# Optimization experiments

Measured on AMD Instinct MI355X. Metric: run time of the kernel, lower is better.

The kernel has to match this reference:

```python
import jax, jax.numpy as jnp
import numpy as np

STEP = 256  # samples per frame index step (start = index * 256)


def setup_inputs() -> dict:
    key = jax.random.key(0)
    ks = jax.random.split(key, 6)
    B, E, N, D, R = 64, 8, 32768, 128, 16
    events = jax.random.normal(ks[0], (B, E, N), dtype=jnp.float32) * 0.1
    indices = jax.random.randint(ks[1], (B, E), 0, N // STEP)  # frame offsets
    g = jax.random.normal(ks[2], (B, D), dtype=jnp.float32)
    rooms = jax.random.normal(ks[3], (R, N), dtype=jnp.float32) * 0.05
    w_room = jax.random.normal(ks[4], (D, R), dtype=jnp.float32) * 0.05
    b_room = jnp.zeros((R,), dtype=jnp.float32)
    w_mix = jax.random.normal(ks[5], (D, 1), dtype=jnp.float32) * 0.05
    b_mix = jnp.zeros((1,), dtype=jnp.float32)
    return {"events": events, "indices": indices, "g": g, "rooms": rooms,
            "w_room": w_room, "b_room": b_room, "w_mix": w_mix, "b_mix": b_mix}


def reference(events, indices, g, rooms, w_room, b_room, w_mix, b_mix):
    B, E, N = events.shape
    # --- dynamic-offset overlap-add scatter into a 2N buffer ---
    starts = indices.astype(jnp.int32) * STEP              # [B, E]
    pos = starts[:, :, None] + jnp.arange(N, dtype=jnp.int32)  # [B, E, N]
    buf = jnp.zeros((B, 2 * N), dtype=events.dtype)
    buf = buf.at[jnp.arange(B)[:, None, None], pos].add(events)
    dry = buf[:, :N]                                        # [B, N]
    # --- neural reverb: softmax room mixture, FFT convolution ---
    room_w = jax.nn.softmax(g @ w_room + b_room, axis=-1)   # [B, R]
    kernel = room_w @ rooms                                 # [B, N]
    L = 2 * N
    wet = jnp.fft.irfft(jnp.fft.rfft(dry, n=L) * jnp.fft.rfft(kernel, n=L), n=L)[:, :N]
    # --- wet/dry mix and peak normalization ---
    mix = jax.nn.sigmoid(g @ w_mix + b_mix)                 # [B, 1]
    out = mix * wet + (1.0 - mix) * dry                     # [B, N]
    out = out[:, None, :]                                   # [B, 1, N]
    mx = jnp.max(out, axis=-1, keepdims=True)
    return out / (mx + 1e-8)
```

## Files before the change

### kernel.cpp

```cpp
#include <hip/hip_runtime.h>
#include <hip/hip_fp16.h>
#include <math.h>

#define N_T 32768
#define L 65536
#define BATCH 64
#define NPAIR 32
#define NEV 8
#define NROOM 16
#define DGATE 128
#define ROWP 258
#define TWP 65
#define TWP2 33
#define TILE 16384
#define TWO_PI 6.2831853071795864769f
#define INV_L (1.0f / 65536.0f)
#define PW_SCALE (1.0f / 256.0f)
#define COL_SCALE (1.0f / 256.0f)

__device__ __forceinline__ float2 cmul(float2 a, float2 b) {
    return make_float2(a.x * b.x - a.y * b.y, a.x * b.y + a.y * b.x);
}
__device__ __forceinline__ int dr4(int p) {
    return ((p & 3) << 6) | ((p & 12) << 2) | ((p & 48) >> 2) | ((p & 192) >> 6);
}

__device__ __forceinline__ void bf4f(float2& a, float2& b, float2& c, float2& d,
                                     const float2* tw, int f, int q) {
    float2 t0 = make_float2(a.x + c.x, a.y + c.y);
    float2 t1 = make_float2(a.x - c.x, a.y - c.y);
    float2 t2 = make_float2(b.x + d.x, b.y + d.y);
    float2 u  = make_float2(b.x - d.x, b.y - d.y);
    float2 t3 = make_float2(u.y, -u.x);
    a = make_float2(t0.x + t2.x, t0.y + t2.y);
    b = cmul(make_float2(t1.x + t3.x, t1.y + t3.y), tw[f * q]);
    c = cmul(make_float2(t0.x - t2.x, t0.y - t2.y), tw[2 * f * q]);
    d = cmul(make_float2(t1.x - t3.x, t1.y - t3.y), tw[3 * f * q]);
}
__device__ __forceinline__ void bf4i(float2& a, float2& b, float2& c, float2& d,
                                     const float2* tw, int f, int q) {
    float2 w1 = tw[f * q], w2 = tw[2 * f * q], w3 = tw[3 * f * q];
    float2 y0 = a;
    float2 y1 = cmul(b, make_float2(w1.x, -w1.y));
    float2 y2 = cmul(c, make_float2(w2.x, -w2.y));
    float2 y3 = cmul(d, make_float2(w3.x, -w3.y));
    float2 t0 = make_float2(y0.x + y2.x, y0.y + y2.y);
    float2 t2 = make_float2(y0.x - y2.x, y0.y - y2.y);
    float2 t1 = make_float2(y1.x + y3.x, y1.y + y3.y);
    float2 u  = make_float2(y1.x - y3.x, y1.y - y3.y);
    a = make_float2(t0.x + t1.x, t0.y + t1.y);
    b = make_float2(t2.x - u.y, t2.y + u.x);
    c = make_float2(t0.x - t1.x, t0.y - t1.y);
    d = make_float2(t2.x + u.y, t2.y - u.x);
}
__device__ __forceinline__ void bfly4_fwd(float2* A, int a0, int st, const float2* tw, int f, int q) {
    bf4f(A[a0], A[a0 + st], A[a0 + 2 * st], A[a0 + 3 * st], tw, f, q);
}
__device__ __forceinline__ void bfly4_inv(float2* A, int a0, int st, const float2* tw, int f, int q) {
    bf4i(A[a0], A[a0 + st], A[a0 + 2 * st], A[a0 + 3 * st], tw, f, q);
}

__global__ __launch_bounds__(1024) void k_fwd(const float* __restrict__ events,
                                              const int* __restrict__ indices,
                                              const float* __restrict__ rooms,
                                              const float* __restrict__ g,
                                              const float* __restrict__ w_room,
                                              const float* __restrict__ b_room,
                                              __half* __restrict__ dryfh,
                                              __half2* __restrict__ C) {
    __shared__ float2 T[128 * TWP];
    __shared__ float2 tw[256];
    __shared__ float2 fine[256];
    __shared__ float wr_s[NROOM];
    int t = threadIdx.x;
    int a = blockIdx.x >> 2;
    int cg = blockIdx.x & 3;
    int c0 = cg * 64;
    __half2* tile = C + ((size_t)(a * 4 + cg)) * TILE;
    if (t < 256) {
        float sv, cv;
        __sincosf(-TWO_PI * (float)t * (1.0f / 256.0f), &sv, &cv);
        tw[t] = make_float2(cv, sv);
        __sincosf(-TWO_PI * (float)t * INV_L, &sv, &cv);
        fine[t] = make_float2(cv, sv);
    }
    if (t >= 256 && t < 256 + NROOM) {
        int r = t - 256;
        const float* gb = g + a * DGATE;
        float acc = b_room[r];
        for (int d = 0; d < DGATE; d++) acc += gb[d] * w_room[d * NROOM + r];
        wr_s[r] = acc;
    }
    __syncthreads();
    if (t == 0) {
        float m = wr_s[0];
        for (int r = 1; r < NROOM; r++) m = fmaxf(m, wr_s[r]);
        float e[NROOM];
        float s = 0.f;
        for (int r = 0; r < NROOM; r++) { e[r] = expf(wr_s[r] - m); s += e[r]; }
        float inv = 1.f / s;
        for (int r = 0; r < NROOM; r++) wr_s[r] = e[r] * inv;
    }
    __syncthreads();
    float* dtile = (float*)T;
    float* ktile = dtile + 128 * 64;
    {
        int n2 = t >> 3;
        int cc = (t & 7) << 3;
        const float* eb = events + (size_t)a * NEV * N_T;
        const int* ib = indices + a * NEV;
        float4 dA = make_float4(0.f, 0.f, 0.f, 0.f), dB = dA;
#pragma unroll
        for (int e = 0; e < NEV; e++) {
            int s = ib[e];
            if (n2 >= s) {
                const float* er = eb + e * N_T + ((n2 - s) << 8) + c0 + cc;
                float4 vA = *(const float4*)er;
                float4 vB = *(const float4*)(er + 4);
                dA.x += vA.x; dA.y += vA.y; dA.z += vA.z; dA.w += vA.w;
                dB.x += vB.x; dB.y += vB.y; dB.z += vB.z; dB.w += vB.w;
            }
        }
        float4 kA = make_float4(0.f, 0.f, 0.f, 0.f), kB = kA;
#pragma unroll
        for (int r = 0; r < NROOM; r++) {
            float w = wr_s[r];
            const float* rr = rooms + (size_t)r * N_T + (n2 << 8) + c0 + cc;
            float4 vA = *(const float4*)rr;
            float4 vB = *(const float4*)(rr + 4);
            kA.x += w * vA.x; kA.y += w * vA.y; kA.z += w * vA.z; kA.w += w * vA.w;
            kB.x += w * vB.x; kB.y += w * vB.y; kB.z += w * vB.z; kB.w += w * vB.w;
        }
        __half2 hd[4];
        hd[0] = __float22half2_rn(make_float2(dA.x, dA.y));
        hd[1] = __float22half2_rn(make_float2(dA.z, dA.w));
        hd[2] = __float22half2_rn(make_float2(dB.x, dB.y));
        hd[3] = __float22half2_rn(make_float2(dB.z, dB.w));
        *(float4*)(dryfh + (size_t)a * N_T + (n2 << 8) + c0 + cc) = *(float4*)hd;
        *(float4*)&dtile[(n2 << 6) + cc] = dA;
        *(float4*)&dtile[(n2 << 6) + cc + 4] = dB;
        *(float4*)&ktile[(n2 << 6) + cc] = kA;
        *(float4*)&ktile[(n2 << 6) + cc + 4] = kB;
    }
    __syncthreads();
    int j = t >> 6, c = t & 63;
    int n1 = c0 + c;
    float2 r[16];
#pragma unroll
    for (int m = 0; m < 8; m++) {
        int n2 = j + 16 * m;
        r[m] = make_float2(dtile[(n2 << 6) + c], ktile[(n2 << 6) + c]);
    }
#pragma unroll
    for (int m = 8; m < 16; m++) r[m] = make_float2(0.f, 0.f);
#pragma unroll
    for (int m0 = 0; m0 < 4; m0++) bf4f(r[m0], r[m0 + 4], r[m0 + 8], r[m0 + 12], tw, 1, j + 16 * m0);
#pragma unroll
    for (int h = 0; h < 4; h++) bf4f(r[4 * h], r[4 * h + 1], r[4 * h + 2], r[4 * h + 3], tw, 4, j);
    __syncthreads();
    float2 r2[16];
#pragma unroll
    for (int m = 0; m < 8; m++) T[(j + 16 * m) * TWP + c] = r[m];
    __syncthreads();
    if (j < 8) {
#pragma unroll
        for (int jj = 0; jj < 16; jj++) r2[jj] = T[(jj + 16 * j) * TWP + c];
    }
    __syncthreads();
#pragma unroll
    for (int m = 8; m < 16; m++) T[(j + 16 * m - 128) * TWP + c] = r[m];
    __syncthreads();
    if (j >= 8) {
#pragma unroll
        for (int jj = 0; jj < 16; jj++) r2[jj] = T[(jj + 16 * (j - 8)) * TWP + c];
    }
#pragma unroll
    for (int q = 0; q < 4; q++) bf4f(r2[q], r2[q + 4], r2[q + 8], r2[q + 12], tw, 16, q);
#pragma unroll
    for (int h = 0; h < 4; h++) bf4f(r2[4 * h], r2[4 * h + 1], r2[4 * h + 2], r2[4 * h + 3], tw, 64, 0);
#pragma unroll
    for (int jj = 0; jj < 16; jj++) {
        int p = jj + 16 * j;
        int k2 = dr4(p);
        int ph = (n1 * k2) & (L - 1);
        float2 w = cmul(tw[ph >> 8], fine[ph & 255]);
        tile[(p << 6) + c] = __float22half2_rn(cmul(r2[jj], w));
    }
}

__device__ __forceinline__ void pw_unit(float2* A, int sJ, int kJ, int sN, int kN) {
    float2 Z0j = A[sJ * ROWP + kJ],       Z0n = A[sN * ROWP + kN];
    float2 Z1j = A[(4 + sJ) * ROWP + kJ], Z1n = A[(4 + sN) * ROWP + kN];
    float2 D0 = make_float2(0.5f * (Z0j.x + Z0n.x), 0.5f * (Z0j.y - Z0n.y));
    float2 K0 = make_float2(0.5f * (Z0j.y + Z0n.y), 0.5f * (Z0n.x - Z0j.x));
    float2 D1 = make_float2(0.5f * (Z1j.x + Z1n.x), 0.5f * (Z1j.y - Z1n.y));
    float2 K1 = make_float2(0.5f * (Z1j.y + Z1n.y), 0.5f * (Z1n.x - Z1j.x));
    float2 W0 = cmul(D0, K0);
    float2 W1 = cmul(D1, K1);
    A[sJ * ROWP + kJ] = make_float2((W0.x - W1.y) * PW_SCALE, (W0.y + W1.x) * PW_SCALE);
    A[sN * ROWP + kN] = make_float2((W0.x + W1.y) * PW_SCALE, (W1.x - W0.y) * PW_SCALE);
}

__global__ void k_rowpw(__half2* __restrict__ C) {
    __shared__ float2 A[8 * ROWP];
    __shared__ float2 tw[192];
    int t = threadIdx.x;
    int p = blockIdx.x >> 6;
    int g = blockIdx.x & 63;
    int rows[4];
    if (g == 0) { rows[0] = 0; rows[1] = 1; rows[2] = 128; rows[3] = 255; }
    else        { rows[0] = 2 * g; rows[1] = 2 * g + 1; rows[2] = 256 - 2 * g; rows[3] = 255 - 2 * g; }
    if (t < 192) {
        float sv, cv;
        __sincosf(-TWO_PI * (float)t * (1.0f / 256.0f), &sv, &cv);
        tw[t] = make_float2(cv, sv);
    }
    __half2* b0 = C + ((size_t)(2 * p) * 4) * TILE;
    __half2* b1 = b0 + 4 * TILE;
    for (int u = t; u < 512; u += 256) {
        int slot = u >> 6;
        int f = (u & 63) << 2;
        int cg = f >> 6, c2 = f & 63;
        const __half2* arr = (slot < 4) ? b0 : b1;
        int grow = dr4(rows[slot & 3]);
        float4 raw = *(const float4*)(arr + cg * TILE + (grow << 6) + c2);
        const __half2* hp = (const __half2*)&raw;
        A[slot * ROWP + f]     = __half22float2(hp[0]);
        A[slot * ROWP + f + 1] = __half22float2(hp[1]);
        A[slot * ROWP + f + 2] = __half22float2(hp[2]);
        A[slot * ROWP + f + 3] = __half22float2(hp[3]);
    }
    __syncthreads();
#pragma unroll
    for (int lm = 8; lm >= 6; lm -= 2) {
        int Q = 1 << (lm - 2), f = 256 >> lm;
        for (int u = t; u < 512; u += 256) {
            int row = u >> 6, qi = u & 63;
            int q = qi & (Q - 1);
            int i0 = ((qi - q) << 2) + q;
            bfly4_fwd(A, row * ROWP + i0, Q, tw, f, q);
        }
        __syncthreads();
    }
#pragma unroll
    for (int lm = 4; lm >= 2; lm -= 2) {
        int Q = 1 << (lm - 2), f = 256 >> lm;
        for (int u = t; u < 512; u += 256) {
            int row = u & 7, qi = u >> 3;
            int q = qi & (Q - 1);
            int i0 = ((qi - q) << 2) + q;
            bfly4_fwd(A, row * ROWP + i0, Q, tw, f, q);
        }
        __syncthreads();
    }
    if (g) {
        pw_unit(A, 0, t, 2, 255 - t);
    } else {
        if (t == 0)      { pw_unit(A, 0, 0, 0, 0); pw_unit(A, 0, 2, 0, 2); }
        else if (t < 128) pw_unit(A, 0, dr4(t), 0, dr4(256 - t));
        else              { int qq = t - 128; pw_unit(A, 2, qq, 2, 255 - qq); }
    }
    pw_unit(A, 1, t, 3, 255 - t);
    __syncthreads();
#pragma unroll
    for (int lm = 2; lm <= 4; lm += 2) {
        int Q = 1 << (lm - 2), f = 256 >> lm;
        int row = t & 3, qi = t >> 2;
        int q = qi & (Q - 1);
        int i0 = ((qi - q) << 2) + q;
        bfly4_inv(A, row * ROWP + i0, Q, tw, f, q);
        __syncthreads();
    }
#pragma unroll
    for (int lm = 6; lm <= 8; lm += 2) {
        int Q = 1 << (lm - 2), f = 256 >> lm;
        int row = t >> 6, qi = t & 63;
        int q = qi & (Q - 1);
        int i0 = ((qi - q) << 2) + q;
        bfly4_inv(A, row * ROWP + i0, Q, tw, f, q);
        __syncthreads();
    }
    {
        int u = t;
        int slot = u >> 6;
        int f = (u & 63) << 2;
        int cg = f >> 6, c2 = f & 63;
        int r = rows[slot];
        __half2 outv[4];
#pragma unroll
        for (int i = 0; i < 4; i++) {
            float2 v = A[slot * ROWP + f + i];
            int ph = ((f + i) * r) & (L - 1);
            float sv, cv;
            __sincosf(TWO_PI * (float)ph * INV_L, &sv, &cv);
            outv[i] = __float22half2_rn(cmul(v, make_float2(cv, sv)));
        }
        *(float4*)(b0 + cg * TILE + (dr4(r) << 6) + c2) = *(float4*)outv;
    }
}

__global__ __launch_bounds__(512) void k_colinv(const __half2* __restrict__ C,
                                                const __half* __restrict__ dryfh,
                                                const float* __restrict__ g,
                                                const float* __restrict__ w_mix,
                                                const float* __restrict__ b_mix,
                                                __half* __restrict__ mixo,
                                                float* __restrict__ partial) {
    __shared__ float2 T[128 * TWP2];
    __shared__ float2 tw[256];
    __shared__ float sm0[8], sm1[8];
    __shared__ float smix[2];
    int t = threadIdx.x;
    int a = blockIdx.x >> 3;
    int cgrp = blockIdx.x & 7;
    int c0 = cgrp * 32;
    const __half2* tile = C + ((size_t)(2 * a * 4 + (c0 >> 6))) * TILE;
    int coff = c0 & 63;
    if (t < 256) {
        float sv, cv;
        __sincosf(-TWO_PI * (float)t * (1.0f / 256.0f), &sv, &cv);
        tw[t] = make_float2(cv, sv);
    }
    if (t >= 256 && t < 258) {
        int bb = 2 * a + (t - 256);
        const float* gb = g + bb * DGATE;
        float acc = b_mix[0];
        for (int d = 0; d < DGATE; d++) acc += gb[d] * w_mix[d];
        smix[t - 256] = 1.f / (1.f + expf(-acc));
    }
    int j = t >> 5, c = t & 31;
    int n1 = c0 + c;
    float2 r[16];
#pragma unroll
    for (int jj = 0; jj < 16; jj++)
        r[jj] = __half22float2(tile[((jj + 16 * j) << 6) + coff + c]);
    __syncthreads();
#pragma unroll
    for (int h = 0; h < 4; h++) bf4i(r[4 * h], r[4 * h + 1], r[4 * h + 2], r[4 * h + 3], tw, 64, 0);
#pragma unroll
    for (int q = 0; q < 4; q++) bf4i(r[q], r[q + 4], r[q + 8], r[q + 12], tw, 16, q);
    float2 r2[16];
    if (j < 8) {
#pragma unroll
        for (int jj = 0; jj < 16; jj++) T[(jj + 16 * j) * TWP2 + c] = r[jj];
    }
    __syncthreads();
#pragma unroll
    for (int m = 0; m < 8; m++) r2[m] = T[(j + 16 * m) * TWP2 + c];
    __syncthreads();
    if (j >= 8) {
#pragma unroll
        for (int jj = 0; jj < 16; jj++) T[(16 * (j - 8) + jj) * TWP2 + c] = r[jj];
    }
    __syncthreads();
#pragma unroll
    for (int m = 8; m < 16; m++) r2[m] = T[(j + 16 * (m - 8)) * TWP2 + c];
#pragma unroll
    for (int h = 0; h < 4; h++) bf4i(r2[4 * h], r2[4 * h + 1], r2[4 * h + 2], r2[4 * h + 3], tw, 4, j);
#pragma unroll
    for (int m0 = 0; m0 < 4; m0++) bf4i(r2[m0], r2[m0 + 4], r2[m0 + 8], r2[m0 + 12], tw, 1, j + 16 * m0);
    int b0 = 2 * a, b1 = 2 * a + 1;
    float mix0 = smix[0], mix1 = smix[1];
    float om0 = 1.f - mix0, om1 = 1.f - mix1;
    const __half* dry0 = dryfh + (size_t)b0 * N_T;
    const __half* dry1 = dryfh + (size_t)b1 * N_T;
    __half* mo0 = mixo + (size_t)b0 * N_T;
    __half* mo1 = mixo + (size_t)b1 * N_T;
    float m0 = -3.4e38f, m1 = -3.4e38f;
#pragma unroll
    for (int m = 0; m < 8; m++) {
        int pos = n1 + ((j + 16 * m) << 8);
        float d0 = __half2float(dry0[pos]), d1 = __half2float(dry1[pos]);
        float o0 = mix0 * (r2[m].x * COL_SCALE) + om0 * d0;
        float o1 = mix1 * (r2[m].y * COL_SCALE) + om1 * d1;
        mo0[pos] = __float2half(o0);
        mo1[pos] = __float2half(o1);
        m0 = fmaxf(m0, o0);
        m1 = fmaxf(m1, o1);
    }
#pragma unroll
    for (int off = 32; off > 0; off >>= 1) {
        m0 = fmaxf(m0, __shfl_down(m0, off));
        m1 = fmaxf(m1, __shfl_down(m1, off));
    }
    if ((t & 63) == 0) { sm0[t >> 6] = m0; sm1[t >> 6] = m1; }
    __syncthreads();
    if (t == 0) {
        float p0 = sm0[0], p1 = sm1[0];
#pragma unroll
        for (int w = 1; w < 8; w++) { p0 = fmaxf(p0, sm0[w]); p1 = fmaxf(p1, sm1[w]); }
        partial[b0 * 8 + cgrp] = p0;
        partial[b1 * 8 + cgrp] = p1;
    }
}

__global__ void k_norm(const __half* __restrict__ mixo, const float* __restrict__ partial,
                       float* __restrict__ out) {
    int blk = blockIdx.x;
    int b = blk >> 5;
    int ch = blk & 31;
    __shared__ float smx;
    if (threadIdx.x < 8) {
        float p = partial[b * 8 + threadIdx.x];
#pragma unroll
        for (int off = 4; off > 0; off >>= 1) p = fmaxf(p, __shfl_down(p, off, 8));
        if (threadIdx.x == 0) smx = p;
    }
    __syncthreads();
    float inv = 1.f / (smx + 1e-8f);
    size_t base = (size_t)b * N_T + ch * 1024 + threadIdx.x * 4;
    float2 hraw = *(const float2*)(mixo + base);
    const __half2* hp = (const __half2*)&hraw;
    float2 v0 = __half22float2(hp[0]);
    float2 v1 = __half22float2(hp[1]);
    float4 o = make_float4(v0.x * inv, v0.y * inv, v1.x * inv, v1.y * inv);
    *(float4*)(out + base) = o;
}

extern "C" void kernel_launch(void* const* d_in, const int* in_sizes, int n_in,
                              void* d_out, int out_size, void* d_ws, size_t ws_size,
                              hipStream_t stream) {
    const float* events = (const float*)d_in[0];
    const int* indices = (const int*)d_in[1];
    const float* g      = (const float*)d_in[2];
    const float* rooms  = (const float*)d_in[3];
    const float* w_room = (const float*)d_in[4];
    const float* b_room = (const float*)d_in[5];
    const float* w_mix  = (const float*)d_in[6];
    const float* b_mix  = (const float*)d_in[7];
    float* out = (float*)d_out;

    char* ws = (char*)d_ws;
    __half2* C = (__half2*)ws;
    size_t off = (size_t)BATCH * L * sizeof(__half2);
    __half* dryfh = (__half*)(ws + off);
    off += (size_t)BATCH * N_T * sizeof(__half);
    __half* mixo = (__half*)(ws + off);
    off += (size_t)BATCH * N_T * sizeof(__half);
    float* partial = (float*)(ws + off);

    k_fwd<<<BATCH * 4, 1024, 0, stream>>>(events, indices, rooms, g, w_room, b_room, dryfh, C);
    k_rowpw<<<NPAIR * 64, 256, 0, stream>>>(C);
    k_colinv<<<NPAIR * 8, 512, 0, stream>>>(C, dryfh, g, w_mix, b_mix, mixo, partial);
    k_norm<<<BATCH * 32, 256, 0, stream>>>(mixo, partial, out);
}
```

Baseline: 56.89 us.

## Split forward FFT into 32-column tiles and parallelize gate dot products

The forward column-FFT kernel now runs twice as many 512-thread blocks, each covering 32 columns instead of 64, and the intermediate tile layout shrinks to 32-wide. The row and inverse kernels are updated to use this layout, so the inverse kernel reads its tile without a column offset. The room-logit and mix-gate dot products are spread across 256 threads as partial sums instead of being done serially by 16 or 2 threads. The events load is also moved ahead of the softmax so it overlaps the gate computation. The aim is better occupancy and shorter serial prologues, at the cost of recomputing the twiddle tables and room softmax in twice as many blocks.

New measurement: 54.36 us (median of 2 runs). -4.4%, faster.

```diff
diff --git a/kernel.cpp b/kernel.cpp
--- a/kernel.cpp
+++ b/kernel.cpp
@@ -10,9 +10,8 @@
 #define NROOM 16
 #define DGATE 128
 #define ROWP 258
-#define TWP 65
-#define TWP2 33
-#define TILE 16384
+#define TP32 33
+#define TILE32 8192
 #define TWO_PI 6.2831853071795864769f
 #define INV_L (1.0f / 65536.0f)
 #define PW_SCALE (1.0f / 256.0f)
@@ -60,56 +59,45 @@
     bf4i(A[a0], A[a0 + st], A[a0 + 2 * st], A[a0 + 3 * st], tw, f, q);
 }
 
-__global__ __launch_bounds__(1024) void k_fwd(const float* __restrict__ events,
-                                              const int* __restrict__ indices,
-                                              const float* __restrict__ rooms,
-                                              const float* __restrict__ g,
-                                              const float* __restrict__ w_room,
-                                              const float* __restrict__ b_room,
-                                              __half* __restrict__ dryfh,
-                                              __half2* __restrict__ C) {
-    __shared__ float2 T[128 * TWP];
+__global__ __launch_bounds__(512) void k_fwd(const float* __restrict__ events,
+                                             const int* __restrict__ indices,
+                                             const float* __restrict__ rooms,
+                                             const float* __restrict__ g,
+                                             const float* __restrict__ w_room,
+                                             const float* __restrict__ b_room,
+                                             __half* __restrict__ dryfh,
+                                             __half2* __restrict__ C) {
+    __shared__ float2 T[128 * TP32];
     __shared__ float2 tw[256];
     __shared__ float2 fine[256];
+    __shared__ float gpart[256];
     __shared__ float wr_s[NROOM];
     int t = threadIdx.x;
-    int a = blockIdx.x >> 2;
-    int cg = blockIdx.x & 3;
-    int c0 = cg * 64;
-    __half2* tile = C + ((size_t)(a * 4 + cg)) * TILE;
+    int a = blockIdx.x >> 3;
+    int cg = blockIdx.x & 7;
+    int c0 = cg * 32;
+    __half2* tile = C + ((size_t)(a * 8 + cg)) * TILE32;
     if (t < 256) {
         float sv, cv;
         __sincosf(-TWO_PI * (float)t * (1.0f / 256.0f), &sv, &cv);
         tw[t] = make_float2(cv, sv);
         __sincosf(-TWO_PI * (float)t * INV_L, &sv, &cv);
         fine[t] = make_float2(cv, sv);
-    }
-    if (t >= 256 && t < 256 + NROOM) {
-        int r = t - 256;
-        const float* gb = g + a * DGATE;
-        float acc = b_room[r];
-        for (int d = 0; d < DGATE; d++) acc += gb[d] * w_room[d * NROOM + r];
-        wr_s[r] = acc;
-    }
-    __syncthreads();
-    if (t == 0) {
-        float m = wr_s[0];
-        for (int r = 1; r < NROOM; r++) m = fmaxf(m, wr_s[r]);
-        float e[NROOM];
-        float s = 0.f;
-        for (int r = 0; r < NROOM; r++) { e[r] = expf(wr_s[r] - m); s += e[r]; }
-        float inv = 1.f / s;
-        for (int r = 0; r < NROOM; r++) wr_s[r] = e[r] * inv;
-    }
-    __syncthreads();
+        int r = t & 15, ch = t >> 4;
+        const float* gb = g + a * DGATE + ch * 8;
+        const float* wr = w_room + ch * 8 * NROOM + r;
+        float acc = 0.f;
+#pragma unroll
+        for (int i = 0; i < 8; i++) acc += gb[i] * wr[i * NROOM];
+        gpart[t] = acc;
+    }
     float* dtile = (float*)T;
-    float* ktile = dtile + 128 * 64;
+    float* ktile = dtile + 128 * 32;
+    int n2 = t >> 2, cc = (t & 3) << 3;
+    float4 dA = make_float4(0.f, 0.f, 0.f, 0.f), dB = dA;
     {
-        int n2 = t >> 3;
-        int cc = (t & 7) << 3;
         const float* eb = events + (size_t)a * NEV * N_T;
         const int* ib = indices + a * NEV;
-        float4 dA = make_float4(0.f, 0.f, 0.f, 0.f), dB = dA;
 #pragma unroll
         for (int e = 0; e < NEV; e++) {
             int s = ib[e];
@@ -121,6 +109,33 @@
                 dB.x += vB.x; dB.y += vB.y; dB.z += vB.z; dB.w += vB.w;
             }
         }
+        __half2 hd[4];
+        hd[0] = __float22half2_rn(make_float2(dA.x, dA.y));
+        hd[1] = __float22half2_rn(make_float2(dA.z, dA.w));
+        hd[2] = __float22half2_rn(make_float2(dB.x, dB.y));
+        hd[3] = __float22half2_rn(make_float2(dB.z, dB.w));
+        *(float4*)(dryfh + (size_t)a * N_T + (n2 << 8) + c0 + cc) = *(float4*)hd;
+        *(float4*)&dtile[(n2 << 5) + cc] = dA;
+        *(float4*)&dtile[(n2 << 5) + cc + 4] = dB;
+    }
+    __syncthreads();
+    if (t < 16) {
+        float s = b_room[t];
+#pragma unroll
+        for (int ch = 0; ch < 16; ch++) s += gpart[ch * 16 + t];
+        wr_s[t] = s;
+    }
+    __syncthreads();
+    if (t == 0) {
+        float m = wr_s[0];
+        for (int r = 1; r < NROOM; r++) m = fmaxf(m, wr_s[r]);
+        float e[NROOM], s = 0.f;
+        for (int r = 0; r < NROOM; r++) { e[r] = expf(wr_s[r] - m); s += e[r]; }
+        float inv = 1.f / s;
+        for (int r = 0; r < NROOM; r++) wr_s[r] = e[r] * inv;
+    }
+    __syncthreads();
+    {
         float4 kA = make_float4(0.f, 0.f, 0.f, 0.f), kB = kA;
 #pragma unroll
         for (int r = 0; r < NROOM; r++) {
@@ -131,25 +146,17 @@
             kA.x += w * vA.x; kA.y += w * vA.y; kA.z += w * vA.z; kA.w += w * vA.w;
             kB.x += w * vB.x; kB.y += w * vB.y; kB.z += w * vB.z; kB.w += w * vB.w;
         }
-        __half2 hd[4];
-        hd[0] = __float22half2_rn(make_float2(dA.x, dA.y));
-        hd[1] = __float22half2_rn(make_float2(dA.z, dA.w));
-        hd[2] = __float22half2_rn(make_float2(dB.x, dB.y));
-        hd[3] = __float22half2_rn(make_float2(dB.z, dB.w));
-        *(float4*)(dryfh + (size_t)a * N_T + (n2 << 8) + c0 + cc) = *(float4*)hd;
-        *(float4*)&dtile[(n2 << 6) + cc] = dA;
-        *(float4*)&dtile[(n2 << 6) + cc + 4] = dB;
-        *(float4*)&ktile[(n2 << 6) + cc] = kA;
-        *(float4*)&ktile[(n2 << 6) + cc + 4] = kB;
-    }
-    __syncthreads();
-    int j = t >> 6, c = t & 63;
+        *(float4*)&ktile[(n2 << 5) + cc] = kA;
+        *(float4*)&ktile[(n2 << 5) + cc + 4] = kB;
+    }
+    __syncthreads();
+    int j = t >> 5, c = t & 31;
     int n1 = c0 + c;
     float2 r[16];
 #pragma unroll
     for (int m = 0; m < 8; m++) {
-        int n2 = j + 16 * m;
-        r[m] = make_float2(dtile[(n2 << 6) + c], ktile[(n2 << 6) + c]);
+        int nn = j + 16 * m;
+        r[m] = make_float2(dtile[(nn << 5) + c], ktile[(nn << 5) + c]);
     }
 #pragma unroll
     for (int m = 8; m < 16; m++) r[m] = make_float2(0.f, 0.f);
@@ -160,19 +167,19 @@
     __syncthreads();
     float2 r2[16];
 #pragma unroll
-    for (int m = 0; m < 8; m++) T[(j + 16 * m) * TWP + c] = r[m];
+    for (int m = 0; m < 8; m++) T[(j + 16 * m) * TP32 + c] = r[m];
     __syncthreads();
     if (j < 8) {
 #pragma unroll
-        for (int jj = 0; jj < 16; jj++) r2[jj] = T[(jj + 16 * j) * TWP + c];
-    }
-    __syncthreads();
-#pragma unroll
-    for (int m = 8; m < 16; m++) T[(j + 16 * m - 128) * TWP + c] = r[m];
+        for (int jj = 0; jj < 16; jj++) r2[jj] = T[(jj + 16 * j) * TP32 + c];
+    }
+    __syncthreads();
+#pragma unroll
+    for (int m = 8; m < 16; m++) T[(j + 16 * m - 128) * TP32 + c] = r[m];
     __syncthreads();
     if (j >= 8) {
 #pragma unroll
-        for (int jj = 0; jj < 16; jj++) r2[jj] = T[(jj + 16 * (j - 8)) * TWP + c];
+        for (int jj = 0; jj < 16; jj++) r2[jj] = T[(jj + 16 * (j - 8)) * TP32 + c];
     }
 #pragma unroll
     for (int q = 0; q < 4; q++) bf4f(r2[q], r2[q + 4], r2[q + 8], r2[q + 12], tw, 16, q);
@@ -184,7 +191,7 @@
         int k2 = dr4(p);
         int ph = (n1 * k2) & (L - 1);
         float2 w = cmul(tw[ph >> 8], fine[ph & 255]);
-        tile[(p << 6) + c] = __float22half2_rn(cmul(r2[jj], w));
+        tile[(p << 5) + c] = __float22half2_rn(cmul(r2[jj], w));
     }
 }
 
@@ -215,15 +222,15 @@
         __sincosf(-TWO_PI * (float)t * (1.0f / 256.0f), &sv, &cv);
         tw[t] = make_float2(cv, sv);
     }
-    __half2* b0 = C + ((size_t)(2 * p) * 4) * TILE;
-    __half2* b1 = b0 + 4 * TILE;
+    __half2* b0 = C + ((size_t)(2 * p) * 8) * TILE32;
+    __half2* b1 = b0 + 8 * TILE32;
     for (int u = t; u < 512; u += 256) {
         int slot = u >> 6;
         int f = (u & 63) << 2;
-        int cg = f >> 6, c2 = f & 63;
+        int cg = f >> 5, c2 = f & 31;
         const __half2* arr = (slot < 4) ? b0 : b1;
         int grow = dr4(rows[slot & 3]);
-        float4 raw = *(const float4*)(arr + cg * TILE + (grow << 6) + c2);
+        float4 raw = *(const float4*)(arr + cg * TILE32 + (grow << 5) + c2);
         const __half2* hp = (const __half2*)&raw;
         A[slot * ROWP + f]     = __half22float2(hp[0]);
         A[slot * ROWP + f + 1] = __half22float2(hp[1]);
@@ -284,7 +291,7 @@
         int u = t;
         int slot = u >> 6;
         int f = (u & 63) << 2;
-        int cg = f >> 6, c2 = f & 63;
+        int cg = f >> 5, c2 = f & 31;
         int r = rows[slot];
         __half2 outv[4];
 #pragma unroll
@@ -295,7 +302,7 @@
             __sincosf(TWO_PI * (float)ph * INV_L, &sv, &cv);
             outv[i] = __float22half2_rn(cmul(v, make_float2(cv, sv)));
         }
-        *(float4*)(b0 + cg * TILE + (dr4(r) << 6) + c2) = *(float4*)outv;
+        *(float4*)(b0 + cg * TILE32 + (dr4(r) << 5) + c2) = *(float4*)outv;
     }
 }
 
@@ -306,35 +313,36 @@
                                                 const float* __restrict__ b_mix,
                                                 __half* __restrict__ mixo,
                                                 float* __restrict__ partial) {
-    __shared__ float2 T[128 * TWP2];
+    __shared__ float2 T[128 * TP32];
     __shared__ float2 tw[256];
+    __shared__ float mpart[256];
     __shared__ float sm0[8], sm1[8];
     __shared__ float smix[2];
     int t = threadIdx.x;
     int a = blockIdx.x >> 3;
     int cgrp = blockIdx.x & 7;
     int c0 = cgrp * 32;
-    const __half2* tile = C + ((size_t)(2 * a * 4 + (c0 >> 6))) * TILE;
-    int coff = c0 & 63;
+    const __half2* tile = C + ((size_t)(2 * a * 8 + cgrp)) * TILE32;
     if (t < 256) {
         float sv, cv;
         __sincosf(-TWO_PI * (float)t * (1.0f / 256.0f), &sv, &cv);
         tw[t] = make_float2(cv, sv);
-    }
-    if (t >= 256 && t < 258) {
-        int bb = 2 * a + (t - 256);
-        const float* gb = g + bb * DGATE;
-        float acc = b_mix[0];
-        for (int d = 0; d < DGATE; d++) acc += gb[d] * w_mix[d];
-        smix[t - 256] = 1.f / (1.f + expf(-acc));
+        int bb = t >> 7, d = t & 127;
+        mpart[t] = g[(2 * a + bb) * DGATE + d] * w_mix[d];
     }
     int j = t >> 5, c = t & 31;
     int n1 = c0 + c;
     float2 r[16];
 #pragma unroll
     for (int jj = 0; jj < 16; jj++)
-        r[jj] = __half22float2(tile[((jj + 16 * j) << 6) + coff + c]);
-    __syncthreads();
+        r[jj] = __half22float2(tile[((jj + 16 * j) << 5) + c]);
+    __syncthreads();
+    if (t < 2) {
+        float acc = b_mix[0];
+#pragma unroll
+        for (int i = 0; i < 128; i++) acc += mpart[(t << 7) + i];
+        smix[t] = 1.f / (1.f + expf(-acc));
+    }
 #pragma unroll
     for (int h = 0; h < 4; h++) bf4i(r[4 * h], r[4 * h + 1], r[4 * h + 2], r[4 * h + 3], tw, 64, 0);
 #pragma unroll
@@ -342,19 +350,19 @@
     float2 r2[16];
     if (j < 8) {
 #pragma unroll
-        for (int jj = 0; jj < 16; jj++) T[(jj + 16 * j) * TWP2 + c] = r[jj];
-    }
-    __syncthreads();
-#pragma unroll
-    for (int m = 0; m < 8; m++) r2[m] = T[(j + 16 * m) * TWP2 + c];
+        for (int jj = 0; jj < 16; jj++) T[(jj + 16 * j) * TP32 + c] = r[jj];
+    }
+    __syncthreads();
+#pragma unroll
+    for (int m = 0; m < 8; m++) r2[m] = T[(j + 16 * m) * TP32 + c];
     __syncthreads();
     if (j >= 8) {
 #pragma unroll
-        for (int jj = 0; jj < 16; jj++) T[(16 * (j - 8) + jj) * TWP2 + c] = r[jj];
-    }
-    __syncthreads();
-#pragma unroll
-    for (int m = 8; m < 16; m++) r2[m] = T[(j + 16 * (m - 8)) * TWP2 + c];
+        for (int jj = 0; jj < 16; jj++) T[(16 * (j - 8) + jj) * TP32 + c] = r[jj];
+    }
+    __syncthreads();
+#pragma unroll
+    for (int m = 8; m < 16; m++) r2[m] = T[(j + 16 * (m - 8)) * TP32 + c];
 #pragma unroll
     for (int h = 0; h < 4; h++) bf4i(r2[4 * h], r2[4 * h + 1], r2[4 * h + 2], r2[4 * h + 3], tw, 4, j);
 #pragma unroll
@@ -439,7 +447,7 @@
     off += (size_t)BATCH * N_T * sizeof(__half);
     float* partial = (float*)(ws + off);
 
-    k_fwd<<<BATCH * 4, 1024, 0, stream>>>(events, indices, rooms, g, w_room, b_room, dryfh, C);
+    k_fwd<<<BATCH * 8, 512, 0, stream>>>(events, indices, rooms, g, w_room, b_room, dryfh, C);
     k_rowpw<<<NPAIR * 64, 256, 0, stream>>>(C);
     k_colinv<<<NPAIR * 8, 512, 0, stream>>>(C, dryfh, g, w_mix, b_mix, mixo, partial);
     k_norm<<<BATCH * 32, 256, 0, stream>>>(mixo, partial, out);
```
